# Performance work log

Hardware: AMD Instinct MI355X
Metric: run time of the kernel (lower is better)

Reference implementation:

```python
import jax, jax.numpy as jnp
import numpy as np

N_NODES = 100000
N_EDGES = 1600000
IN_DIM = 128
HID = 128
OUT_DIM = 64
N_GRAPHS = 128
BN_EPS = 1e-5


def _bn(h, gamma, beta):
    # training-mode BatchNorm1d: biased batch statistics over the node axis
    mu = jnp.mean(h, axis=0)
    var = jnp.mean(jnp.square(h - mu), axis=0)
    return gamma * (h - mu) * jax.lax.rsqrt(var + BN_EPS) + beta


def _gcn(h, W, b, src, dst, norm, n):
    # GCNConv: x @ W, symmetric-normalized scatter-add aggregation, + bias
    h = h @ W                                   # [N, F_out]
    msg = h[src] * norm[:, None]                # gather per edge (incl. self-loops)
    agg = jax.ops.segment_sum(msg, dst, num_segments=n)
    return agg + b


def setup_inputs() -> dict:
    key = jax.random.key(0)
    ks = jax.random.split(key, 24)
    x = jax.random.normal(ks[0], (N_NODES, IN_DIM), dtype=jnp.float32)
    edge_index = jax.random.randint(ks[1], (2, N_EDGES), 0, N_NODES, dtype=jnp.int32)
    batch = jnp.sort(jax.random.randint(ks[2], (N_NODES,), 0, N_GRAPHS, dtype=jnp.int32))
    dims = [(IN_DIM, HID), (HID, HID), (HID, HID), (HID, OUT_DIM)]
    inp = {"x": x, "edge_index": edge_index, "batch": batch}
    for i, (fi, fo) in enumerate(dims):
        inp[f"W{i}"] = jax.random.normal(ks[3 + i], (fi, fo), dtype=jnp.float32) / np.sqrt(fi)
        inp[f"b{i}"] = jnp.zeros((fo,), dtype=jnp.float32)
        inp[f"g{i}"] = jnp.ones((fo,), dtype=jnp.float32)
        inp[f"be{i}"] = jnp.zeros((fo,), dtype=jnp.float32)
    inp["skip_weight"] = jnp.float32(0.1)
    return inp


def reference(x, edge_index, batch,
              W0, b0, g0, be0, W1, b1, g1, be1,
              W2, b2, g2, be2, W3, b3, g3, be3, skip_weight):
    n = x.shape[0]
    loops = jnp.arange(n, dtype=edge_index.dtype)
    src = jnp.concatenate([edge_index[0], loops])
    dst = jnp.concatenate([edge_index[1], loops])
    deg = jax.ops.segment_sum(jnp.ones_like(src, dtype=x.dtype), dst, num_segments=n)
    dinv = jax.lax.rsqrt(jnp.maximum(deg, 1.0))  # deg >= 1 due to self-loops
    norm = dinv[src] * dinv[dst]

    # layer 0 (dropout is identity in eval reference)
    h = jax.nn.relu(_bn(_gcn(x, W0, b0, src, dst, norm, n), g0, be0))
    # middle layers with skip connections
    for W, b, g, be in ((W1, b1, g1, be1), (W2, b2, g2, be2)):
        h_prev = h
        h = jax.nn.relu(_bn(_gcn(h, W, b, src, dst, norm, n), g, be))
        h = h + skip_weight * h_prev
    # final layer, no relu
    h = _bn(_gcn(h, W3, b3, src, dst, norm, n), g3, be3)

    # global mean pool over graphs
    sums = jax.ops.segment_sum(h, batch, num_segments=N_GRAPHS)
    cnts = jax.ops.segment_sum(jnp.ones((n,), dtype=h.dtype), batch, num_segments=N_GRAPHS)
    return sums / jnp.maximum(cnts, 1.0)[:, None]
```

## Files before the change

### kernel.cpp

```cpp
#include <hip/hip_runtime.h>


typedef unsigned short u16;
typedef unsigned int u32;
typedef __attribute__((ext_vector_type(8))) short bf16x8;
typedef __attribute__((ext_vector_type(2))) unsigned int u32x2;
typedef __attribute__((ext_vector_type(4))) float f32x4;

__device__ __forceinline__ float bflo(u32 u) { return __uint_as_float(u << 16); }
__device__ __forceinline__ float bfhi(u32 u) { return __uint_as_float(u & 0xffff0000u); }
__device__ __forceinline__ u16 f2bf(float f) {
    u32 u = __float_as_uint(f);
    u32 r = u + 0x7fffu + ((u >> 16) & 1u);
    return (u16)(r >> 16);
}
__device__ __forceinline__ u32 pack2(float a, float b) {
    return (u32)f2bf(a) | ((u32)f2bf(b) << 16);
}


__global__ void k_deg(const int* __restrict__ edst, int E, int* __restrict__ deg) {
    int e = blockIdx.x * blockDim.x + threadIdx.x;
    if (e < E) atomicAdd(&deg[edst[e]], 1);
}

__global__ void k_dinv(const int* __restrict__ deg, int n, float* __restrict__ dinv) {
    int i = blockIdx.x * blockDim.x + threadIdx.x;
    if (i < n) {
        int c = deg[i] + 1;
        dinv[i] = rsqrtf((float)c);
    }
}

__global__ void k_bsum(const int* __restrict__ deg, int n, int* __restrict__ bsum) {
    __shared__ int sd[256];
    int base = blockIdx.x * 1024;
    int end = base + 1024; if (end > n) end = n;
    int s = 0;
    for (int i = base + threadIdx.x; i < end; i += 256) s += deg[i] + 1;
    sd[threadIdx.x] = s;
    __syncthreads();
    for (int off = 128; off > 0; off >>= 1) {
        if (threadIdx.x < off) sd[threadIdx.x] += sd[threadIdx.x + off];
        __syncthreads();
    }
    if (threadIdx.x == 0) bsum[blockIdx.x] = sd[0];
}

__global__ void k_scanb(int* __restrict__ bsum, int B) {
    int run = 0;
    for (int i = 0; i < B; ++i) { int v = bsum[i]; bsum[i] = run; run += v; }
}

__global__ void k_offs(const int* __restrict__ deg, int n, const int* __restrict__ bsum,
                       int* __restrict__ offs) {
    __shared__ int sd[256];
    int base = blockIdx.x * 1024;
    int carry = bsum[blockIdx.x];
    for (int tile = 0; tile < 4; ++tile) {
        int i = base + tile * 256 + threadIdx.x;
        int v = (i < n) ? (deg[i] + 1) : 0;
        sd[threadIdx.x] = v;
        __syncthreads();
        int x = v;
        for (int off = 1; off < 256; off <<= 1) {
            int y = (threadIdx.x >= off) ? sd[threadIdx.x - off] : 0;
            __syncthreads();
            x += y;
            sd[threadIdx.x] = x;
            __syncthreads();
        }
        if (i < n) offs[i] = carry + x - v;
        if (i == n - 1) offs[n] = carry + x;
        carry += sd[255];
        __syncthreads();
    }
}

__global__ void k_fill_edges(const int* __restrict__ esrc, const int* __restrict__ edst,
                             int E, const float* __restrict__ dinv,
                             const int* __restrict__ offs, int* __restrict__ deg,
                             uint2* __restrict__ csre) {
    int e = blockIdx.x * blockDim.x + threadIdx.x;
    if (e < E) {
        int s = esrc[e], d = edst[e];
        int rank = atomicSub(&deg[d], 1) - 1;
        u32x2 val;
        val.x = (u32)s;
        val.y = __float_as_uint(dinv[s] * dinv[d]);
        __builtin_nontemporal_store(val, (u32x2*)&csre[offs[d] + rank]);
    }
}

__global__ void k_fill_self(int n, const float* __restrict__ dinv,
                            const int* __restrict__ offs, uint2* __restrict__ csre) {
    int i = blockIdx.x * blockDim.x + threadIdx.x;
    if (i < n) {
        float dv = dinv[i];
        csre[offs[i + 1] - 1] = make_uint2((u32)i, __float_as_uint(dv * dv));
    }
}

__global__ void k_gcnt_bs(const int* __restrict__ batch, int n, int* __restrict__ gcnt) {
    int g = threadIdx.x;
    if (g < 128) {
        int lo0 = 0, hi0 = n;
        while (lo0 < hi0) { int m = (lo0 + hi0) >> 1; if (batch[m] < g) lo0 = m + 1; else hi0 = m; }
        int lo1 = lo0, hi1 = n;
        while (lo1 < hi1) { int m = (lo1 + hi1) >> 1; if (batch[m] < g + 1) lo1 = m + 1; else hi1 = m; }
        gcnt[g] = lo1 - lo0;
    }
}


template <int FOUT>
__global__ void k_wt(const float* __restrict__ W, u16* __restrict__ Wt) {
    __shared__ u16 l[128 * (FOUT + 8)];
    for (int i = threadIdx.x; i < 128 * FOUT; i += 256) {
        int k = i / FOUT, nn = i % FOUT;
        l[k * (FOUT + 8) + nn] = f2bf(W[i]);
    }
    __syncthreads();
    for (int i = threadIdx.x; i < 128 * FOUT; i += 256) {
        int nn = i >> 7, k = i & 127;
        Wt[nn * 128 + k] = l[k * (FOUT + 8) + nn];
    }
}


template <int FOUT, int MODE, bool STOREH>
__global__ __launch_bounds__(256) void k_gemm_mfma(const void* __restrict__ Ap,
                                                   const u16* __restrict__ hprev,
                                                   const float* __restrict__ coef,
                                                   const float* __restrict__ swp,
                                                   const u16* __restrict__ Wt,
                                                   u16* __restrict__ hout,
                                                   u16* __restrict__ O, int n) {
    constexpr int NT = FOUT / 16;
    const int lane = threadIdx.x & 63;
    const int wave = threadIdx.x >> 6;
    const int fr = lane & 15;
    const int fq = lane >> 4;
    const int rowbase = blockIdx.x * 64 + wave * 16;
    const int arow = rowbase + fr;
    const bool aok = arow < n;
    const float* af = (const float*)Ap + (size_t)arow * 128 + fq * 8;
    const u16* hp = (MODE == 3) ? hprev + (size_t)arow * 128 + fq * 8 : nullptr;
    const u16* wp = Wt + fr * 128 + fq * 8;
    float sw = 0.f;
    if constexpr (MODE == 3) sw = *swp;

    f32x4 acc[NT];
#pragma unroll
    for (int t = 0; t < NT; ++t)
#pragma unroll
        for (int q = 0; q < 4; ++q) acc[t][q] = 0.f;

#pragma unroll
    for (int kk = 0; kk < 4; ++kk) {
        bf16x8 a;
#pragma unroll
        for (int q = 0; q < 8; ++q) a[q] = 0;
        if (aok) {
            if constexpr (MODE == 1) {
                const float4 x0 = *(const float4*)(af + kk * 32);
                const float4 x1 = *(const float4*)(af + kk * 32 + 4);
                a[0] = (short)f2bf(x0.x); a[1] = (short)f2bf(x0.y);
                a[2] = (short)f2bf(x0.z); a[3] = (short)f2bf(x0.w);
                a[4] = (short)f2bf(x1.x); a[5] = (short)f2bf(x1.y);
                a[6] = (short)f2bf(x1.z); a[7] = (short)f2bf(x1.w);
            } else {
                const int k0 = kk * 32 + fq * 8;
                const float4 v0 = *(const float4*)(af + kk * 32);
                const float4 v1 = *(const float4*)(af + kk * 32 + 4);
                const float4 sc0 = *(const float4*)&coef[k0];
                const float4 sc1 = *(const float4*)&coef[k0 + 4];
                const float4 sh0 = *(const float4*)&coef[128 + k0];
                const float4 sh1 = *(const float4*)&coef[128 + k0 + 4];
                float r[8];
                r[0] = fmaxf(fmaf(v0.x, sc0.x, sh0.x), 0.f);
                r[1] = fmaxf(fmaf(v0.y, sc0.y, sh0.y), 0.f);
                r[2] = fmaxf(fmaf(v0.z, sc0.z, sh0.z), 0.f);
                r[3] = fmaxf(fmaf(v0.w, sc0.w, sh0.w), 0.f);
                r[4] = fmaxf(fmaf(v1.x, sc1.x, sh1.x), 0.f);
                r[5] = fmaxf(fmaf(v1.y, sc1.y, sh1.y), 0.f);
                r[6] = fmaxf(fmaf(v1.z, sc1.z, sh1.z), 0.f);
                r[7] = fmaxf(fmaf(v1.w, sc1.w, sh1.w), 0.f);
                if constexpr (MODE == 3) {
                    const uint4 pv = *(const uint4*)(hp + kk * 32);
                    r[0] = fmaf(sw, bflo(pv.x), r[0]); r[1] = fmaf(sw, bfhi(pv.x), r[1]);
                    r[2] = fmaf(sw, bflo(pv.y), r[2]); r[3] = fmaf(sw, bfhi(pv.y), r[3]);
                    r[4] = fmaf(sw, bflo(pv.z), r[4]); r[5] = fmaf(sw, bfhi(pv.z), r[5]);
                    r[6] = fmaf(sw, bflo(pv.w), r[6]); r[7] = fmaf(sw, bfhi(pv.w), r[7]);
                }
                uint4 o;
                o.x = pack2(r[0], r[1]);
                o.y = pack2(r[2], r[3]);
                o.z = pack2(r[4], r[5]);
                o.w = pack2(r[6], r[7]);
                a = *(const bf16x8*)&o;
                if constexpr (STOREH)
                    *(uint4*)&hout[(size_t)arow * 128 + k0] = o;
            }
        }
#pragma unroll
        for (int t = 0; t < NT; ++t) {
            bf16x8 b = *(const bf16x8*)(wp + t * 16 * 128 + kk * 32);
            acc[t] = __builtin_amdgcn_mfma_f32_16x16x32_bf16(a, b, acc[t], 0, 0, 0);
        }
    }
#pragma unroll
    for (int i = 0; i < 4; ++i) {
        const int row = rowbase + fq * 4 + i;
        if (row < n) {
#pragma unroll
            for (int t = 0; t < NT; ++t)
                O[(size_t)row * FOUT + t * 16 + fr] = f2bf(acc[t][i]);
        }
    }
}


template <int F>
__global__ __launch_bounds__(256) void k_agg(const u16* __restrict__ hW,
                                             const uint2* __restrict__ csre,
                                             const int* __restrict__ offs,
                                             float* __restrict__ agg, int n) {
    constexpr int TPN = F / 8;
    constexpr int NPB = 256 / TPN;
    const int lane = threadIdx.x % TPN;
    const int sub = threadIdx.x / TPN;
    const int fbase = lane * 8;

    for (int node = blockIdx.x * NPB + sub; node < n; node += gridDim.x * NPB) {
        const int beg = offs[node];
        const int end = offs[node + 1];
        float4 b0 = make_float4(0.f, 0.f, 0.f, 0.f);
        float4 b1 = make_float4(0.f, 0.f, 0.f, 0.f);
        float4 c0 = make_float4(0.f, 0.f, 0.f, 0.f);
        float4 c1 = make_float4(0.f, 0.f, 0.f, 0.f);
        int j = beg;
        for (; j + 8 <= end; j += 8) {
            uint2 ei[8];
#pragma unroll
            for (int q = 0; q < 8; ++q) ei[q] = csre[j + q];
            uint4 v[8];
#pragma unroll
            for (int q = 0; q < 8; ++q)
                v[q] = *(const uint4*)&hW[(size_t)ei[q].x * F + fbase];
#pragma unroll
            for (int q = 0; q < 8; ++q) {
                const float w = __uint_as_float(ei[q].y);
                if (q & 1) {
                    c0.x = fmaf(bflo(v[q].x), w, c0.x); c0.y = fmaf(bfhi(v[q].x), w, c0.y);
                    c0.z = fmaf(bflo(v[q].y), w, c0.z); c0.w = fmaf(bfhi(v[q].y), w, c0.w);
                    c1.x = fmaf(bflo(v[q].z), w, c1.x); c1.y = fmaf(bfhi(v[q].z), w, c1.y);
                    c1.z = fmaf(bflo(v[q].w), w, c1.z); c1.w = fmaf(bfhi(v[q].w), w, c1.w);
                } else {
                    b0.x = fmaf(bflo(v[q].x), w, b0.x); b0.y = fmaf(bfhi(v[q].x), w, b0.y);
                    b0.z = fmaf(bflo(v[q].y), w, b0.z); b0.w = fmaf(bfhi(v[q].y), w, b0.w);
                    b1.x = fmaf(bflo(v[q].z), w, b1.x); b1.y = fmaf(bfhi(v[q].z), w, b1.y);
                    b1.z = fmaf(bflo(v[q].w), w, b1.z); b1.w = fmaf(bfhi(v[q].w), w, b1.w);
                }
            }
        }
        for (; j < end; ++j) {
            const uint2 e0 = csre[j];
            const float w = __uint_as_float(e0.y);
            const uint4 v0 = *(const uint4*)&hW[(size_t)e0.x * F + fbase];
            b0.x = fmaf(bflo(v0.x), w, b0.x); b0.y = fmaf(bfhi(v0.x), w, b0.y);
            b0.z = fmaf(bflo(v0.y), w, b0.z); b0.w = fmaf(bfhi(v0.y), w, b0.w);
            b1.x = fmaf(bflo(v0.z), w, b1.x); b1.y = fmaf(bfhi(v0.z), w, b1.y);
            b1.z = fmaf(bflo(v0.w), w, b1.z); b1.w = fmaf(bfhi(v0.w), w, b1.w);
        }
        b0.x += c0.x; b0.y += c0.y; b0.z += c0.z; b0.w += c0.w;
        b1.x += c1.x; b1.y += c1.y; b1.z += c1.z; b1.w += c1.w;
        __builtin_nontemporal_store(*(const f32x4*)&b0,
                                    (f32x4*)&agg[(size_t)node * F + fbase]);
        __builtin_nontemporal_store(*(const f32x4*)&b1,
                                    (f32x4*)&agg[(size_t)node * F + fbase + 4]);
    }
}


template <int F>
__global__ __launch_bounds__(256) void k_stats(const float* __restrict__ aggf,
                                               float* __restrict__ stats,
                                               int* __restrict__ ticket,
                                               const float* __restrict__ g,
                                               const float* __restrict__ be,
                                               float* __restrict__ coef,
                                               float inv_n, int n8) {
    constexpr int TPR = F / 8;
    const int tid0 = blockIdx.x * 256 + threadIdx.x;
    float s[8], q[8];
#pragma unroll
    for (int k = 0; k < 8; ++k) { s[k] = 0.f; q[k] = 0.f; }
    for (int i = tid0; i < n8; i += gridDim.x * 256) {
        const float4 v0 = *(const float4*)&aggf[(size_t)i * 8];
        const float4 v1 = *(const float4*)&aggf[(size_t)i * 8 + 4];
        s[0] += v0.x; s[1] += v0.y; s[2] += v0.z; s[3] += v0.w;
        s[4] += v1.x; s[5] += v1.y; s[6] += v1.z; s[7] += v1.w;
        q[0] = fmaf(v0.x, v0.x, q[0]); q[1] = fmaf(v0.y, v0.y, q[1]);
        q[2] = fmaf(v0.z, v0.z, q[2]); q[3] = fmaf(v0.w, v0.w, q[3]);
        q[4] = fmaf(v1.x, v1.x, q[4]); q[5] = fmaf(v1.y, v1.y, q[5]);
        q[6] = fmaf(v1.z, v1.z, q[6]); q[7] = fmaf(v1.w, v1.w, q[7]);
    }
#pragma unroll
    for (int m = TPR; m < 64; m <<= 1) {
#pragma unroll
        for (int k = 0; k < 8; ++k) {
            s[k] += __shfl_xor(s[k], m);
            q[k] += __shfl_xor(q[k], m);
        }
    }
    __shared__ float sred[2][4][TPR * 8];
    const int w = threadIdx.x >> 6;
    const int l64 = threadIdx.x & 63;
    if (l64 < TPR) {
#pragma unroll
        for (int k = 0; k < 8; ++k) {
            sred[0][w][l64 * 8 + k] = s[k];
            sred[1][w][l64 * 8 + k] = q[k];
        }
    }
    __syncthreads();
    if (threadIdx.x < TPR * 8) {
        float a = sred[0][0][threadIdx.x] + sred[0][1][threadIdx.x] +
                  sred[0][2][threadIdx.x] + sred[0][3][threadIdx.x];
        float b = sred[1][0][threadIdx.x] + sred[1][1][threadIdx.x] +
                  sred[1][2][threadIdx.x] + sred[1][3][threadIdx.x];
        const int ff = threadIdx.x & (F - 1);
        atomicAdd(&stats[ff], a);
        atomicAdd(&stats[F + ff], b);
    }
    __threadfence();
    __shared__ int last;
    if (threadIdx.x == 0) last = (atomicAdd(ticket, 1) == (int)gridDim.x - 1) ? 1 : 0;
    __syncthreads();
    if (last) {
        if (threadIdx.x < F) {
            const int f = threadIdx.x;
            float sum = atomicAdd(&stats[f], 0.f);
            float ssq = atomicAdd(&stats[F + f], 0.f);
            float mean = sum * inv_n;
            float var = fmaxf(ssq * inv_n - mean * mean, 0.f);
            float sc = g[f] * rsqrtf(var + 1e-5f);
            coef[f] = sc;
            coef[F + f] = be[f] - mean * sc;
        }
    }
}


__global__ __launch_bounds__(256) void k_bnpool(const float* __restrict__ C,
                                                const int* __restrict__ batch,
                                                const float* __restrict__ coef,
                                                float* __restrict__ out, int n,
                                                int chunk) {
    __shared__ float pool[128 * 64];
    for (int i = threadIdx.x; i < 128 * 64; i += 256) pool[i] = 0.f;
    __syncthreads();
    const int f = threadIdx.x & 63;
    const int sub = threadIdx.x >> 6;
    const float sc = coef[f];
    const float sh = coef[64 + f];
    const int lo = blockIdx.x * chunk;
    int hi = lo + chunk; if (hi > n) hi = n;
    for (int node = lo + sub; node < hi; node += 4) {
        float v = fmaf(sc, C[(size_t)node * 64 + f], sh);
        int g = batch[node];
        atomicAdd(&pool[g * 64 + f], v);
    }
    __syncthreads();
    for (int i = threadIdx.x; i < 128 * 64; i += 256) {
        float v = pool[i];
        if (v != 0.f) atomicAdd(&out[i], v);
    }
}

__global__ void k_div(float* __restrict__ out, const int* __restrict__ gcnt, int total) {
    int i = blockIdx.x * blockDim.x + threadIdx.x;
    if (i < total) {
        int g = i >> 6;
        int c = gcnt[g];
        if (c < 1) c = 1;
        out[i] = out[i] / (float)c;
    }
}


static inline size_t align256(size_t x) { return (x + 255) & ~(size_t)255; }

extern "C" void kernel_launch(void* const* d_in, const int* in_sizes, int n_in,
                              void* d_out, int out_size, void* d_ws, size_t ws_size,
                              hipStream_t stream) {
    const float* x    = (const float*)d_in[0];
    const int* ei     = (const int*)d_in[1];
    const int* batch  = (const int*)d_in[2];
    const float* W0   = (const float*)d_in[3];
    const float* g0   = (const float*)d_in[5];
    const float* be0  = (const float*)d_in[6];
    const float* W1   = (const float*)d_in[7];
    const float* g1   = (const float*)d_in[9];
    const float* be1  = (const float*)d_in[10];
    const float* W2   = (const float*)d_in[11];
    const float* g2   = (const float*)d_in[13];
    const float* be2  = (const float*)d_in[14];
    const float* W3   = (const float*)d_in[15];
    const float* g3   = (const float*)d_in[17];
    const float* be3  = (const float*)d_in[18];
    const float* swp  = (const float*)d_in[19];

    const int N = in_sizes[0] / 128;
    const int E = in_sizes[1] / 2;
    const int T = E + N;
    const int* esrc = ei;
    const int* edst = ei + E;

    char* p = (char*)d_ws;
    auto carve = [&](size_t bytes) -> char* {
        char* r = p;
        p += align256(bytes);
        return r;
    };
    int*   deg    = (int*)carve((size_t)N * 4);
    float* dinv   = (float*)carve((size_t)N * 4);
    int*   offs   = (int*)carve((size_t)(N + 1) * 4);
    int*   bsum   = (int*)carve(256 * 4);
    uint2* csre   = (uint2*)carve((size_t)T * 8);
    float* stats  = (float*)carve(4 * 256 * 4);
    float* coef   = (float*)carve(4 * 256 * 4);
    int*   ticket = (int*)carve(4 * 4);
    int*   gcnt   = (int*)carve(128 * 4);
    u16*   Wt0    = (u16*)carve(128 * 128 * 2);
    u16*   Wt1    = (u16*)carve(128 * 128 * 2);
    u16*   Wt2    = (u16*)carve(128 * 128 * 2);
    u16*   Wt3    = (u16*)carve(64 * 128 * 2);
    u16*   h0     = (u16*)carve((size_t)N * 128 * 2);
    u16*   h1     = (u16*)carve((size_t)N * 128 * 2);
    u16*   hWb    = (u16*)carve((size_t)N * 128 * 2);
    float* aggf   = (float*)carve((size_t)N * 128 * 4);

    hipMemsetAsync(deg, 0, (size_t)N * 4, stream);
    hipMemsetAsync(stats, 0, 4 * 256 * 4, stream);
    hipMemsetAsync(ticket, 0, 4 * 4, stream);
    hipMemsetAsync(d_out, 0, (size_t)out_size * 4, stream);

    const int EB = (E + 255) / 256;
    const int NB = (N + 255) / 256;
    const int B = (N + 1023) / 1024;
    k_deg<<<EB, 256, 0, stream>>>(edst, E, deg);
    k_dinv<<<NB, 256, 0, stream>>>(deg, N, dinv);
    k_bsum<<<B, 256, 0, stream>>>(deg, N, bsum);
    k_scanb<<<1, 1, 0, stream>>>(bsum, B);
    k_offs<<<B, 256, 0, stream>>>(deg, N, bsum, offs);
    k_fill_self<<<NB, 256, 0, stream>>>(N, dinv, offs, csre);
    k_fill_edges<<<EB, 256, 0, stream>>>(esrc, edst, E, dinv, offs, deg, csre);
    k_gcnt_bs<<<1, 128, 0, stream>>>(batch, N, gcnt);

    k_wt<128><<<1, 256, 0, stream>>>(W0, Wt0);
    k_wt<128><<<1, 256, 0, stream>>>(W1, Wt1);
    k_wt<128><<<1, 256, 0, stream>>>(W2, Wt2);
    k_wt<64><<<1, 256, 0, stream>>>(W3, Wt3);

    const float inv_n = 1.0f / (float)N;
    const int gemm_grid = (N + 63) / 64;
    const int chunk = (N + 255) / 256;
    const int n8_128 = N * 16;
    const int n8_64 = N * 8;

    k_gemm_mfma<128, 1, false><<<gemm_grid, 256, 0, stream>>>(
        (const void*)x, nullptr, nullptr, nullptr, Wt0, nullptr, hWb, N);
    k_agg<128><<<2048, 256, 0, stream>>>(hWb, csre, offs, aggf, N);
    k_stats<128><<<256, 256, 0, stream>>>(aggf, stats + 0, ticket + 0, g0, be0,
                                          coef + 0, inv_n, n8_128);
    k_gemm_mfma<128, 2, true><<<gemm_grid, 256, 0, stream>>>(
        (const void*)aggf, nullptr, coef + 0, nullptr, Wt1, h0, hWb, N);
    k_agg<128><<<2048, 256, 0, stream>>>(hWb, csre, offs, aggf, N);
    k_stats<128><<<256, 256, 0, stream>>>(aggf, stats + 256, ticket + 1, g1, be1,
                                          coef + 256, inv_n, n8_128);
    k_gemm_mfma<128, 3, true><<<gemm_grid, 256, 0, stream>>>(
        (const void*)aggf, h0, coef + 256, swp, Wt2, h1, hWb, N);
    k_agg<128><<<2048, 256, 0, stream>>>(hWb, csre, offs, aggf, N);
    k_stats<128><<<256, 256, 0, stream>>>(aggf, stats + 512, ticket + 2, g2, be2,
                                          coef + 512, inv_n, n8_128);
    k_gemm_mfma<64, 3, false><<<gemm_grid, 256, 0, stream>>>(
        (const void*)aggf, h1, coef + 512, swp, Wt3, nullptr, hWb, N);
    k_agg<64><<<2048, 256, 0, stream>>>(hWb, csre, offs, aggf, N);
    k_stats<64><<<256, 256, 0, stream>>>(aggf, stats + 768, ticket + 3, g3, be3,
                                         coef + 768, inv_n, n8_64);
    k_bnpool<<<256, 256, 0, stream>>>(aggf, batch, coef + 768, (float*)d_out, N, chunk);
    k_div<<<(out_size + 255) / 256, 256, 0, stream>>>((float*)d_out, gcnt, out_size);
}
```

Before: 790.5 us.

## Partition CSR edge fill by destination range to localize scattered writes

Replaces the one-thread-per-edge CSR fill with a partitioned fill. Each block scans one segment of the edge list and handles only edges whose destination falls in its 8192-node partition. Atomics and CSR writes then land in a compact address range that can stay cache-resident, instead of scattering across the whole array. The cost is that edst is read P times (about 13 here), and the nontemporal store is dropped.

```diff
diff --git a/kernel.cpp b/kernel.cpp
--- a/kernel.cpp
+++ b/kernel.cpp
@@ -4,8 +4,9 @@
 typedef unsigned short u16;
 typedef unsigned int u32;
 typedef __attribute__((ext_vector_type(8))) short bf16x8;
-typedef __attribute__((ext_vector_type(2))) unsigned int u32x2;
 typedef __attribute__((ext_vector_type(4))) float f32x4;
+
+#define PSH 13
 
 __device__ __forceinline__ float bflo(u32 u) { return __uint_as_float(u << 16); }
 __device__ __forceinline__ float bfhi(u32 u) { return __uint_as_float(u & 0xffff0000u); }
@@ -77,18 +78,22 @@
     }
 }
 
-__global__ void k_fill_edges(const int* __restrict__ esrc, const int* __restrict__ edst,
-                             int E, const float* __restrict__ dinv,
-                             const int* __restrict__ offs, int* __restrict__ deg,
-                             uint2* __restrict__ csre) {
-    int e = blockIdx.x * blockDim.x + threadIdx.x;
-    if (e < E) {
-        int s = esrc[e], d = edst[e];
-        int rank = atomicSub(&deg[d], 1) - 1;
-        u32x2 val;
-        val.x = (u32)s;
-        val.y = __float_as_uint(dinv[s] * dinv[d]);
-        __builtin_nontemporal_store(val, (u32x2*)&csre[offs[d] + rank]);
+__global__ void k_fillp(const int* __restrict__ esrc, const int* __restrict__ edst,
+                        int E, const float* __restrict__ dinv,
+                        const int* __restrict__ offs, int* __restrict__ deg,
+                        uint2* __restrict__ csre, int P, int segsz) {
+    const int p = blockIdx.x % P;
+    const int seg = blockIdx.x / P;
+    const int lo = seg * segsz;
+    int hi = lo + segsz; if (hi > E) hi = E;
+    for (int e = lo + threadIdx.x; e < hi; e += 256) {
+        const int d = edst[e];
+        if ((d >> PSH) == p) {
+            const int s = esrc[e];
+            const int rank = atomicSub(&deg[d], 1) - 1;
+            csre[offs[d] + rank] =
+                make_uint2((u32)s, __float_as_uint(dinv[s] * dinv[d]));
+        }
     }
 }
 
@@ -450,13 +455,17 @@
     const int EB = (E + 255) / 256;
     const int NB = (N + 255) / 256;
     const int B = (N + 1023) / 1024;
+    const int P = (N + (1 << PSH) - 1) >> PSH;
+    const int NSEG = 160;
+    const int segsz = (E + NSEG - 1) / NSEG;
     k_deg<<<EB, 256, 0, stream>>>(edst, E, deg);
     k_dinv<<<NB, 256, 0, stream>>>(deg, N, dinv);
     k_bsum<<<B, 256, 0, stream>>>(deg, N, bsum);
     k_scanb<<<1, 1, 0, stream>>>(bsum, B);
     k_offs<<<B, 256, 0, stream>>>(deg, N, bsum, offs);
     k_fill_self<<<NB, 256, 0, stream>>>(N, dinv, offs, csre);
-    k_fill_edges<<<EB, 256, 0, stream>>>(esrc, edst, E, dinv, offs, deg, csre);
+    k_fillp<<<NSEG * P, 256, 0, stream>>>(esrc, edst, E, dinv, offs, deg, csre,
+                                          P, segsz);
     k_gcnt_bs<<<1, 128, 0, stream>>>(batch, N, gcnt);
 
     k_wt<128><<<1, 256, 0, stream>>>(W0, Wt0);
```

New measurement: 805.2 us. Within noise of the previous version (+1.9%).
